# Optimization experiments

Measured on AMD Instinct MI355X. Metric: run time of the kernel, lower is better.

Reference implementation:

```python
import jax, jax.numpy as jnp
import numpy as np

N_HEADS, D_MODEL, DK, DV = 16, 1024, 64, 64
B, S = 4, 2048


def setup_inputs() -> dict:
    key = jax.random.key(0)
    ks = jax.random.split(key, 7)
    scale = 1.0 / np.sqrt(D_MODEL)
    return {
        "Q": jax.random.normal(ks[0], (B, S, D_MODEL), dtype=jnp.float32),
        "K": jax.random.normal(ks[1], (B, S, D_MODEL), dtype=jnp.float32),
        "V": jax.random.normal(ks[2], (B, S, D_MODEL), dtype=jnp.float32),
        # Linear weights stored as [in, out] so y = x @ W (equivalent to torch x @ W.T)
        "w_q": jax.random.normal(ks[3], (D_MODEL, N_HEADS * DK), dtype=jnp.float32) * scale,
        "w_k": jax.random.normal(ks[4], (D_MODEL, N_HEADS * DK), dtype=jnp.float32) * scale,
        "w_v": jax.random.normal(ks[5], (D_MODEL, N_HEADS * DV), dtype=jnp.float32) * scale,
        "w_o": jax.random.normal(ks[6], (N_HEADS * DV, D_MODEL), dtype=jnp.float32) * scale,
    }


def reference(Q, K, V, w_q, w_k, w_v, w_o):
    b, s, _ = Q.shape
    # projections -> [B, H, S, d]
    q = (Q @ w_q).reshape(b, s, N_HEADS, DK).transpose(0, 2, 1, 3)
    k = (K @ w_k).reshape(b, s, N_HEADS, DK).transpose(0, 2, 1, 3)
    v = (V @ w_v).reshape(b, s, N_HEADS, DV).transpose(0, 2, 1, 3)
    # scaled dot-product attention, full [B,H,S,S] scores (matches source)
    scores = jnp.einsum("bhqd,bhkd->bhqk", q, k) / jnp.sqrt(jnp.float32(DK))
    attn = jax.nn.softmax(scores, axis=-1)
    x = jnp.einsum("bhqk,bhkd->bhqd", attn, v)
    x = x.transpose(0, 2, 1, 3).reshape(b, s, N_HEADS * DV)
    return x @ w_o
```

## Files before the change

kernel.cpp:

```cpp
#include <hip/hip_runtime.h>
#include <stdint.h>

#define B_   4
#define S_   2048
#define H_   16
#define D_   64
#define DM_  1024
#define NTOK (B_ * S_)

typedef __attribute__((ext_vector_type(8))) short short8;
typedef __attribute__((ext_vector_type(4))) float floatx4;

__device__ inline unsigned short f2bf(float f) {
  unsigned int u = __float_as_uint(f);
  u += 0x7FFFu + ((u >> 16) & 1u);
  return (unsigned short)(u >> 16);
}

__device__ inline floatx4 mfma_bf16(short8 a, short8 b, floatx4 c) {
  return __builtin_amdgcn_mfma_f32_16x16x32_bf16(a, b, c, 0, 0, 0);
}

__device__ inline unsigned int pack_bf2(float lo, float hi) {
  return __builtin_amdgcn_perm(__float_as_uint(hi), __float_as_uint(lo), 0x07060302u);
}

__device__ inline void gload_lds16(const unsigned short* g, unsigned short* l) {
  __builtin_amdgcn_global_load_lds(
      (const __attribute__((address_space(1))) unsigned int*)g,
      (__attribute__((address_space(3))) unsigned int*)l, 16, 0, 0);
}

__global__ __launch_bounds__(256) void cast_bf16_kernel(const float* __restrict__ in,
                                                        unsigned short* __restrict__ out,
                                                        int n4) {
  int i = blockIdx.x * 256 + threadIdx.x;
  if (i < n4) {
    float4 v = ((const float4*)in)[i];
    ushort4 o;
    o.x = f2bf(v.x); o.y = f2bf(v.y); o.z = f2bf(v.z); o.w = f2bf(v.w);
    ((ushort4*)out)[i] = o;
  }
}

__global__ __launch_bounds__(256) void wt_kernel(const float* __restrict__ w0,
                                                 const float* __restrict__ w1,
                                                 const float* __restrict__ w2,
                                                 const float* __restrict__ w3,
                                                 unsigned short* __restrict__ o0,
                                                 unsigned short* __restrict__ o1,
                                                 unsigned short* __restrict__ o2,
                                                 unsigned short* __restrict__ o3) {
  __shared__ unsigned short T[64 * 68];
  const float* w = blockIdx.z == 0 ? w0 : blockIdx.z == 1 ? w1 : blockIdx.z == 2 ? w2 : w3;
  unsigned short* o = blockIdx.z == 0 ? o0 : blockIdx.z == 1 ? o1 : blockIdx.z == 2 ? o2 : o3;
  const int tid = threadIdx.x;
  const int R0 = blockIdx.y * 64;
  const int C0 = blockIdx.x * 64;
  for (int it = 0; it < 16; it++) {
    int lr = it * 4 + (tid >> 6), lc = tid & 63;
    T[lc * 68 + lr] = f2bf(w[(size_t)(R0 + lr) * 1024 + C0 + lc]);
  }
  __syncthreads();
  for (int it = 0; it < 2; it++) {
    int orow = it * 32 + (tid >> 3), oc = (tid & 7) * 8;
    union { ushort4 h[2]; short8 v8; } u;
    u.h[0] = *(const ushort4*)(T + orow * 68 + oc);
    u.h[1] = *(const ushort4*)(T + orow * 68 + oc + 4);
    *(short8*)(o + (size_t)(C0 + orow) * 1024 + R0 + oc) = u.v8;
  }
}

template <int MODE>
__global__ __launch_bounds__(256) void gemm_bt_kernel(const unsigned short* __restrict__ A,
                                                      const unsigned short* __restrict__ BT,
                                                      void* __restrict__ Cout,
                                                      float scale) {
  constexpr int K = 1024;
  __shared__ unsigned short As[128 * 32];
  __shared__ unsigned short Bs[128 * 32];

  const int tid  = threadIdx.x;
  const int wave = tid >> 6, lane = tid & 63;
  const int quad = lane >> 4, l16 = lane & 15;
  const int wm = wave >> 1, wn = wave & 1;
  const int m0 = blockIdx.y * 128, n0 = blockIdx.x * 128;

  floatx4 acc[4][4] = {};

  for (int k0 = 0; k0 < K; k0 += 32) {
    for (int p = 0; p < 2; p++) {
      int i = p * 256 + wave * 64 + lane;
      int row = i >> 2, c = i & 3;
      gload_lds16(A  + (size_t)(m0 + row) * K + k0 + c * 8,
                  As + (size_t)(p * 256 + wave * 64) * 8);
      gload_lds16(BT + (size_t)(n0 + row) * K + k0 + c * 8,
                  Bs + (size_t)(p * 256 + wave * 64) * 8);
    }
    __syncthreads();

    short8 af[4], bfr[4];
    for (int f = 0; f < 4; f++) {
      af[f]  = *(const short8*)(As + (wm * 64 + f * 16 + l16) * 32 + quad * 8);
      bfr[f] = *(const short8*)(Bs + (wn * 64 + f * 16 + l16) * 32 + quad * 8);
    }
    for (int fm = 0; fm < 4; fm++)
      for (int fn = 0; fn < 4; fn++)
        acc[fm][fn] = mfma_bf16(af[fm], bfr[fn], acc[fm][fn]);
    __syncthreads();
  }

  for (int fm = 0; fm < 4; fm++)
    for (int fn = 0; fn < 4; fn++)
      for (int r = 0; r < 4; r++) {
        int gm = m0 + wm * 64 + fm * 16 + quad * 4 + r;
        int gn = n0 + wn * 64 + fn * 16 + l16;
        float val = acc[fm][fn][r] * scale;
        if (MODE == 0) {
          int b = gm >> 11, s = gm & 2047;
          int h = gn >> 6,  d = gn & 63;
          ((unsigned short*)Cout)[((size_t)((b * H_ + h) * S_ + s) << 6) + d] = f2bf(val);
        } else if (MODE == 1) {
          ((float*)Cout)[((size_t)gm << 10) + gn] = val;
        } else {
          int b = gm >> 11, s = gm & 2047;
          int h = gn >> 6,  d = gn & 63;
          int p = ((s & 63) >> 4) + (s & 15) * 4;
          ((unsigned short*)Cout)[(((size_t)(b * H_ + h) * 64 + d) << 11) + (s & ~63) + p] = f2bf(val);
        }
      }
}

__global__ __launch_bounds__(512, 4) void attn_kernel(const unsigned short* __restrict__ q,
                                                      const unsigned short* __restrict__ k,
                                                      const unsigned short* __restrict__ vT,
                                                      unsigned short* __restrict__ X) {
  __shared__ unsigned short Ks[64 * 64];
  __shared__ unsigned short Vt[64 * 64];
  __shared__ unsigned short Ps[8][16 * 72];

  const int tid  = threadIdx.x;
  const int wave = tid >> 6, lane = tid & 63;
  const int quad = lane >> 4, l16 = lane & 15;
  const int bh = blockIdx.x * 8 + (blockIdx.y >> 3);
  const int q0 = (blockIdx.y & 7) * 256;

  const unsigned short* qh = q  + (size_t)bh * S_ * 64;
  const unsigned short* kh = k  + (size_t)bh * S_ * 64;
  const unsigned short* vh = vT + (size_t)bh * 64 * S_;

  short8 qf[2][2];
  for (int qt = 0; qt < 2; qt++) {
    int row = q0 + wave * 32 + qt * 16 + l16;
    for (int kk = 0; kk < 2; kk++)
      qf[qt][kk] = *(const short8*)(qh + (size_t)row * 64 + kk * 32 + quad * 8);
  }

  short8 onesb = {};
  if (l16 == 0)
    for (int e = 0; e < 8; e++) onesb[e] = (short)0x3F80;

  floatx4 O[2][4] = {};
  floatx4 lacc[2] = {};

  for (int j0 = 0; j0 < S_; j0 += 64) {
    __syncthreads();

    {
      int r  = tid >> 3;
      int gc = (tid & 7) ^ (r & 7);
      gload_lds16(kh + (size_t)(j0 + r) * 64 + gc * 8,
                  Ks + (size_t)(wave * 64) * 8);
      gload_lds16(vh + (size_t)r * S_ + j0 + gc * 8,
                  Vt + (size_t)(wave * 64) * 8);
    }
    __syncthreads();

    short8 kf[4][2];
    for (int jf = 0; jf < 4; jf++)
      for (int kk = 0; kk < 2; kk++) {
        int sl = (kk * 4 + quad) ^ (l16 & 7);
        kf[jf][kk] = *(const short8*)(Ks + (jf * 16 + l16) * 64 + sl * 8);
      }

    unsigned short* pw = Ps[wave];
    short8 pa[2][2];
    for (int qt = 0; qt < 2; qt++) {
      floatx4 s[4] = {};
      for (int jf = 0; jf < 4; jf++) {
        s[jf] = mfma_bf16(qf[qt][0], kf[jf][0], s[jf]);
        s[jf] = mfma_bf16(qf[qt][1], kf[jf][1], s[jf]);
      }
      for (int r = 0; r < 4; r++) {
        float e0 = exp2f(s[0][r]), e1 = exp2f(s[1][r]);
        float e2 = exp2f(s[2][r]), e3 = exp2f(s[3][r]);
        uint2 pk;
        pk.x = pack_bf2(e0, e1);
        pk.y = pack_bf2(e2, e3);
        *(uint2*)(pw + (quad * 4 + r) * 72 + l16 * 4) = pk;
      }
      pa[qt][0] = *(const short8*)(pw + l16 * 72 + quad * 8);
      pa[qt][1] = *(const short8*)(pw + l16 * 72 + 32 + quad * 8);
      lacc[qt] = mfma_bf16(pa[qt][0], onesb, lacc[qt]);
      lacc[qt] = mfma_bf16(pa[qt][1], onesb, lacc[qt]);
    }

    for (int df = 0; df < 4; df++) {
      int sl0 = quad ^ (l16 & 7);
      int sl1 = (4 + quad) ^ (l16 & 7);
      short8 v0 = *(const short8*)(Vt + (df * 16 + l16) * 64 + sl0 * 8);
      short8 v1 = *(const short8*)(Vt + (df * 16 + l16) * 64 + sl1 * 8);
      for (int qt = 0; qt < 2; qt++) {
        O[qt][df] = mfma_bf16(pa[qt][0], v0, O[qt][df]);
        O[qt][df] = mfma_bf16(pa[qt][1], v1, O[qt][df]);
      }
    }
  }

  const int b = bh >> 4, h = bh & 15;
  for (int qt = 0; qt < 2; qt++)
    for (int r = 0; r < 4; r++) {
      float lsum = __shfl(lacc[qt][r], (lane & 48));
      float inv = 1.0f / lsum;
      int row = q0 + wave * 32 + qt * 16 + quad * 4 + r;
      unsigned short* dst = X + ((size_t)(b * S_ + row) << 10) + h * 64;
      for (int df = 0; df < 4; df++)
        dst[df * 16 + l16] = f2bf(O[qt][df][r] * inv);
    }
}

extern "C" void kernel_launch(void* const* d_in, const int* in_sizes, int n_in,
                              void* d_out, int out_size, void* d_ws, size_t ws_size,
                              hipStream_t stream) {
  const float* Q  = (const float*)d_in[0];
  const float* K  = (const float*)d_in[1];
  const float* V  = (const float*)d_in[2];
  const float* wq = (const float*)d_in[3];
  const float* wk = (const float*)d_in[4];
  const float* wv = (const float*)d_in[5];
  const float* wo = (const float*)d_in[6];

  char* ws = (char*)d_ws;
  unsigned short* buf0 = (unsigned short*)ws;
  unsigned short* wqT  = (unsigned short*)(ws + (size_t)(16 << 20));
  unsigned short* wkT  = (unsigned short*)(ws + (size_t)(18 << 20));
  unsigned short* wvT  = (unsigned short*)(ws + (size_t)(20 << 20));
  unsigned short* woT  = (unsigned short*)(ws + (size_t)(22 << 20));
  unsigned short* qP   = (unsigned short*)(ws + (size_t)(24 << 20));
  unsigned short* kP   = (unsigned short*)(ws + (size_t)(40 << 20));
  unsigned short* vTg  = (unsigned short*)(ws + (size_t)(56 << 20));

  const int n4 = NTOK * DM_ / 4;
  const float SC = 0.18033688011112043f;

  wt_kernel<<<dim3(16, 16, 4), dim3(256), 0, stream>>>(wq, wk, wv, wo, wqT, wkT, wvT, woT);

  cast_bf16_kernel<<<dim3(8192), dim3(256), 0, stream>>>(Q, buf0, n4);
  gemm_bt_kernel<0><<<dim3(8, 64), dim3(256), 0, stream>>>(buf0, wqT, qP, SC);
  cast_bf16_kernel<<<dim3(8192), dim3(256), 0, stream>>>(K, buf0, n4);
  gemm_bt_kernel<0><<<dim3(8, 64), dim3(256), 0, stream>>>(buf0, wkT, kP, 1.0f);
  cast_bf16_kernel<<<dim3(8192), dim3(256), 0, stream>>>(V, buf0, n4);
  gemm_bt_kernel<2><<<dim3(8, 64), dim3(256), 0, stream>>>(buf0, wvT, vTg, 1.0f);

  attn_kernel<<<dim3(8, 64), dim3(512), 0, stream>>>(qP, kP, vTg, buf0);

  gemm_bt_kernel<1><<<dim3(8, 64), dim3(256), 0, stream>>>(buf0, woT, (float*)d_out, 1.0f);
}
```

Measured before the change: 371.7 us.

## Double-buffer K/V tiles in attention and swizzle GEMM block mapping

The attention kernel now keeps two LDS buffers for K and V. It prefetches the next 64-key tile while computing on the current one, which drops one __syncthreads per iteration and hides global-load latency behind the MFMA and softmax work. The GEMM kernel remaps block indices so consecutive blocks share A row-panels, aiming for better L2 reuse. Smaller tweaks: the first score MFMA accumulates from a constant zero, and exp2f is replaced by the raw hardware exp2 builtin. The extra LDS for double buffering may lower occupancy, and the raw exp2 skips denormal handling.

```diff
diff --git a/kernel.cpp b/kernel.cpp
--- a/kernel.cpp
+++ b/kernel.cpp
@@ -84,7 +84,9 @@
   const int wave = tid >> 6, lane = tid & 63;
   const int quad = lane >> 4, l16 = lane & 15;
   const int wm = wave >> 1, wn = wave & 1;
-  const int m0 = blockIdx.y * 128, n0 = blockIdx.x * 128;
+  const int mb = blockIdx.x * 8 + (blockIdx.y >> 3);
+  const int nb = blockIdx.y & 7;
+  const int m0 = mb * 128, n0 = nb * 128;
 
   floatx4 acc[4][4] = {};
 
@@ -135,8 +137,8 @@
                                                       const unsigned short* __restrict__ k,
                                                       const unsigned short* __restrict__ vT,
                                                       unsigned short* __restrict__ X) {
-  __shared__ unsigned short Ks[64 * 64];
-  __shared__ unsigned short Vt[64 * 64];
+  __shared__ unsigned short Ks[2][64 * 64];
+  __shared__ unsigned short Vt[2][64 * 64];
   __shared__ unsigned short Ps[8][16 * 72];
 
   const int tid  = threadIdx.x;
@@ -149,6 +151,9 @@
   const unsigned short* kh = k  + (size_t)bh * S_ * 64;
   const unsigned short* vh = vT + (size_t)bh * 64 * S_;
 
+  const int sr  = tid >> 3;
+  const int sgc = (tid & 7) ^ (sr & 7);
+
   short8 qf[2][2];
   for (int qt = 0; qt < 2; qt++) {
     int row = q0 + wave * 32 + qt * 16 + l16;
@@ -160,40 +165,45 @@
   if (l16 == 0)
     for (int e = 0; e < 8; e++) onesb[e] = (short)0x3F80;
 
+  const floatx4 fz = {};
   floatx4 O[2][4] = {};
   floatx4 lacc[2] = {};
 
+  gload_lds16(kh + (size_t)sr * 64 + sgc * 8,       Ks[0] + (size_t)(wave * 64) * 8);
+  gload_lds16(vh + (size_t)sr * S_ + 0 + sgc * 8,   Vt[0] + (size_t)(wave * 64) * 8);
+
+  int cur = 0;
   for (int j0 = 0; j0 < S_; j0 += 64) {
     __syncthreads();
 
-    {
-      int r  = tid >> 3;
-      int gc = (tid & 7) ^ (r & 7);
-      gload_lds16(kh + (size_t)(j0 + r) * 64 + gc * 8,
-                  Ks + (size_t)(wave * 64) * 8);
-      gload_lds16(vh + (size_t)r * S_ + j0 + gc * 8,
-                  Vt + (size_t)(wave * 64) * 8);
-    }
-    __syncthreads();
+    if (j0 + 64 < S_) {
+      int nxt = cur ^ 1;
+      gload_lds16(kh + (size_t)(j0 + 64 + sr) * 64 + sgc * 8,
+                  Ks[nxt] + (size_t)(wave * 64) * 8);
+      gload_lds16(vh + (size_t)sr * S_ + (j0 + 64) + sgc * 8,
+                  Vt[nxt] + (size_t)(wave * 64) * 8);
+    }
 
     short8 kf[4][2];
     for (int jf = 0; jf < 4; jf++)
       for (int kk = 0; kk < 2; kk++) {
         int sl = (kk * 4 + quad) ^ (l16 & 7);
-        kf[jf][kk] = *(const short8*)(Ks + (jf * 16 + l16) * 64 + sl * 8);
+        kf[jf][kk] = *(const short8*)(Ks[cur] + (jf * 16 + l16) * 64 + sl * 8);
       }
 
     unsigned short* pw = Ps[wave];
     short8 pa[2][2];
     for (int qt = 0; qt < 2; qt++) {
-      floatx4 s[4] = {};
+      floatx4 s[4];
       for (int jf = 0; jf < 4; jf++) {
-        s[jf] = mfma_bf16(qf[qt][0], kf[jf][0], s[jf]);
+        s[jf] = mfma_bf16(qf[qt][0], kf[jf][0], fz);
         s[jf] = mfma_bf16(qf[qt][1], kf[jf][1], s[jf]);
       }
       for (int r = 0; r < 4; r++) {
-        float e0 = exp2f(s[0][r]), e1 = exp2f(s[1][r]);
-        float e2 = exp2f(s[2][r]), e3 = exp2f(s[3][r]);
+        float e0 = __builtin_amdgcn_exp2f(s[0][r]);
+        float e1 = __builtin_amdgcn_exp2f(s[1][r]);
+        float e2 = __builtin_amdgcn_exp2f(s[2][r]);
+        float e3 = __builtin_amdgcn_exp2f(s[3][r]);
         uint2 pk;
         pk.x = pack_bf2(e0, e1);
         pk.y = pack_bf2(e2, e3);
@@ -208,13 +218,14 @@
     for (int df = 0; df < 4; df++) {
       int sl0 = quad ^ (l16 & 7);
       int sl1 = (4 + quad) ^ (l16 & 7);
-      short8 v0 = *(const short8*)(Vt + (df * 16 + l16) * 64 + sl0 * 8);
-      short8 v1 = *(const short8*)(Vt + (df * 16 + l16) * 64 + sl1 * 8);
+      short8 v0 = *(const short8*)(Vt[cur] + (df * 16 + l16) * 64 + sl0 * 8);
+      short8 v1 = *(const short8*)(Vt[cur] + (df * 16 + l16) * 64 + sl1 * 8);
       for (int qt = 0; qt < 2; qt++) {
         O[qt][df] = mfma_bf16(pa[qt][0], v0, O[qt][df]);
         O[qt][df] = mfma_bf16(pa[qt][1], v1, O[qt][df]);
       }
     }
+    cur ^= 1;
   }
 
   const int b = bh >> 4, h = bh & 15;
```

Result: faster. 340.7 us (-8.3%).
